# Optimization experiments

Measured on AMD Instinct MI355X. Metric: run time of the kernel, lower is better.

Reference implementation:

```python
import jax, jax.numpy as jnp
import numpy as np

N = 8192
TD, ID, D = 768, 1024, 1024
E = 8
GH = D // 2  # gate hidden
EPS = 1e-5


def _init_linear(key, fan_in, shape):
    # torch nn.Linear default init: U(-1/sqrt(fan_in), 1/sqrt(fan_in))
    bound = 1.0 / np.sqrt(fan_in)
    return jax.random.uniform(key, shape, jnp.float32, -bound, bound)


def setup_inputs() -> dict:
    key = jax.random.key(0)
    ks = jax.random.split(key, 16)
    return {
        "text_features": jax.random.normal(ks[0], (N, TD), jnp.float32),
        "image_features": jax.random.normal(ks[1], (N, ID), jnp.float32),
        "Wt": _init_linear(ks[2], TD, (TD, D)),
        "bt": _init_linear(ks[3], TD, (D,)),
        "Wi": _init_linear(ks[4], ID, (ID, D)),
        "bi": _init_linear(ks[5], ID, (D,)),
        "eW1": _init_linear(ks[6], 2 * D, (E, 2 * D, D)),
        "eb1": _init_linear(ks[7], 2 * D, (E, D)),
        "eW2": _init_linear(ks[8], D, (E, D, D)),
        "eb2": _init_linear(ks[9], D, (E, D)),
        "ln_g": jnp.ones((E, D), jnp.float32),
        "ln_b": jnp.zeros((E, D), jnp.float32),
        "gW1": _init_linear(ks[10], 2 * D, (2 * D, GH)),
        "gb1": _init_linear(ks[11], 2 * D, (GH,)),
        "gW2": _init_linear(ks[12], GH, (GH, E)),
        "gb2": _init_linear(ks[13], GH, (E,)),
    }


def reference(text_features, image_features, Wt, bt, Wi, bi,
              eW1, eb1, eW2, eb2, ln_g, ln_b, gW1, gb1, gW2, gb2):
    # project both modalities to shared dim D (dropout is identity in eval)
    ta = text_features @ Wt + bt            # [N, D]
    ia = image_features @ Wi + bi           # [N, D]
    c = jnp.concatenate([ta, ia], axis=-1)  # [N, 2D]

    # gating MLP -> softmax over experts
    gh = jax.nn.silu(c @ gW1 + gb1)                      # [N, GH]
    w = jax.nn.softmax(gh @ gW2 + gb2, axis=-1)          # [N, E]

    # all experts densely, batched over E
    h = jax.nn.silu(jnp.einsum('nc,ecd->ned', c, eW1) + eb1)   # [N, E, D]
    o = jnp.einsum('ned,edf->nef', h, eW2) + eb2               # [N, E, D]

    # per-expert LayerNorm over last dim
    mu = o.mean(axis=-1, keepdims=True)
    var = ((o - mu) ** 2).mean(axis=-1, keepdims=True)
    o = (o - mu) * jax.lax.rsqrt(var + EPS) * ln_g + ln_b      # [N, E, D]

    # gate-weighted sum over experts
    return jnp.einsum('ned,ne->nd', o, w)                      # [N, D]
```

## Files before the change

kernel.cpp:

```cpp
#include <hip/hip_runtime.h>

#define NROWS 8192
#define TDIM 768
#define IDIM 1024
#define DDIM 1024
#define NEXP 8
#define GHID 512

typedef __attribute__((ext_vector_type(8))) short short8;
typedef __attribute__((ext_vector_type(4))) float f4;
typedef __attribute__((ext_vector_type(4))) unsigned short us4;

__device__ __forceinline__ unsigned short f2bf(float f) {
  union { float f; unsigned u; } v; v.f = f;
  unsigned r = v.u + 0x7FFF + ((v.u >> 16) & 1);
  return (unsigned short)(r >> 16);
}
__device__ __forceinline__ float bf2f(unsigned short u) {
  union { unsigned u; float f; } v; v.u = ((unsigned)u) << 16;
  return v.f;
}

__device__ __forceinline__ void gload16(const void* g, void* l) {
  __builtin_amdgcn_global_load_lds(
      (const __attribute__((address_space(1))) void*)g,
      (__attribute__((address_space(3))) void*)l, 16, 0, 0);
}

__global__ __launch_bounds__(256) void cast_bf16_kernel(
    const float* __restrict__ src, unsigned short* __restrict__ dst, int n4) {
  int i = blockIdx.x * 256 + threadIdx.x;
  if (i < n4) {
    f4 v = ((const f4*)src)[i];
    us4 o;
    o[0] = f2bf(v[0]); o[1] = f2bf(v[1]); o[2] = f2bf(v[2]); o[3] = f2bf(v[3]);
    ((us4*)dst)[i] = o;
  }
}

__global__ __launch_bounds__(256) void transpose_cast_kernel(
    const float* __restrict__ src, unsigned short* __restrict__ dst, int R, int C) {
  __shared__ float tile[32][33];
  size_t base = (size_t)blockIdx.z * R * C;
  int c0 = blockIdx.x * 32, r0 = blockIdx.y * 32;
  int tx = threadIdx.x, ty = threadIdx.y;
#pragma unroll
  for (int j = 0; j < 32; j += 8)
    tile[ty + j][tx] = src[base + (size_t)(r0 + ty + j) * C + c0 + tx];
  __syncthreads();
#pragma unroll
  for (int j = 0; j < 32; j += 8)
    dst[base + (size_t)(c0 + ty + j) * R + r0 + tx] = f2bf(tile[tx][ty + j]);
}

template <int SILU, int OUTBF>
__global__ __launch_bounds__(512, 1) void gemm256_kernel(
    const unsigned short* __restrict__ A, const unsigned short* __restrict__ BT,
    const float* __restrict__ bias, void* __restrict__ Cptr,
    int K, int lda, int ldb, int ldc,
    size_t sA, size_t sB, size_t sBias, size_t sC) {
  __shared__ __align__(16) char LDS[131072];

  const unsigned short* Ab = A + (size_t)blockIdx.z * sA;
  const unsigned short* Bb = BT + (size_t)blockIdx.z * sB;
  const float* biasb = bias + (size_t)blockIdx.z * sBias;

  const int gx = gridDim.x;
  const int nwg = gx * gridDim.y;
  const int orig = blockIdx.y * gx + blockIdx.x;
  const int q = nwg >> 3, r = nwg & 7;
  const int xcd = orig & 7, idx = orig >> 3;
  const int wgid = (xcd < r ? xcd * (q + 1) : r * (q + 1) + (xcd - r) * q) + idx;
  const int bx = wgid % gx, by = wgid / gx;

  const int tid = threadIdx.x;
  const int wave = tid >> 6, lane = tid & 63;
  const int wm = wave >> 2, wn = wave & 3;
  const int row0 = by * 256, col0 = bx * 256;

  f4 acc[8][4] = {};

  const int srow = tid >> 3;
  const int scolg = ((tid & 7) << 4) ^ (((tid >> 3) & 7) << 4);
  const size_t lda2 = (size_t)lda * 2, ldb2 = (size_t)ldb * 2;
  const char* Abytes = (const char*)Ab;
  const char* Bbytes = (const char*)Bb;
  const size_t aG = (size_t)(row0 + srow) * lda2 + scolg;
  const size_t bG = (size_t)(col0 + srow) * ldb2 + scolg;
  char* ldsw = LDS + wave * 1024;

  const int aBase = (wm * 128 + (lane & 15)) * 128;
  const int bBase = 32768 + (wn * 64 + (lane & 15)) * 128;
  const int ck0 = ((lane >> 4) << 4) ^ ((lane & 7) << 4);

  const int NT = K >> 6;

#pragma unroll
  for (int p = 0; p < 4; p++)
    gload16(Abytes + aG + (size_t)(p * 64) * lda2, ldsw + p * 8192);
#pragma unroll
  for (int p = 0; p < 4; p++)
    gload16(Bbytes + bG + (size_t)(p * 64) * ldb2, ldsw + 32768 + p * 8192);

  short8 bv[4][2];
  for (int t = 0; t < NT; t++) {
    const int buf = (t & 1) << 16;
    const int nbuf = 65536 - buf;
    const size_t kb = (size_t)(t + 1) << 7;
    const bool more = (t + 1 < NT);

    if (more) {
      gload16(Abytes + aG + kb, ldsw + nbuf);
      gload16(Abytes + aG + (size_t)64 * lda2 + kb, ldsw + nbuf + 8192);
      asm volatile("s_waitcnt vmcnt(2)" ::: "memory");
    } else {
      asm volatile("s_waitcnt vmcnt(0)" ::: "memory");
    }
    __builtin_amdgcn_s_barrier();
    __builtin_amdgcn_sched_barrier(0);
    {
      short8 av[2][2];
#pragma unroll
      for (int n = 0; n < 4; n++)
#pragma unroll
        for (int kk = 0; kk < 2; kk++)
          bv[n][kk] = *(const short8*)(LDS + buf + bBase + n * 2048 + (ck0 ^ (kk << 6)));
#pragma unroll
      for (int m = 0; m < 2; m++)
#pragma unroll
        for (int kk = 0; kk < 2; kk++)
          av[m][kk] = *(const short8*)(LDS + buf + aBase + m * 2048 + (ck0 ^ (kk << 6)));
      asm volatile("s_waitcnt lgkmcnt(0)" ::: "memory");
      __builtin_amdgcn_sched_barrier(0);
      __builtin_amdgcn_s_setprio(1);
#pragma unroll
      for (int kk = 0; kk < 2; kk++)
#pragma unroll
        for (int m = 0; m < 2; m++)
#pragma unroll
          for (int n = 0; n < 4; n++)
            acc[m][n] = __builtin_amdgcn_mfma_f32_16x16x32_bf16(av[m][kk], bv[n][kk], acc[m][n], 0, 0, 0);
      __builtin_amdgcn_s_setprio(0);
    }
    __builtin_amdgcn_s_barrier();

#pragma unroll
    for (int ph = 1; ph < 4; ph++) {
      if (more) {
        if (ph == 1) {
          gload16(Abytes + aG + (size_t)128 * lda2 + kb, ldsw + nbuf + 16384);
          gload16(Abytes + aG + (size_t)192 * lda2 + kb, ldsw + nbuf + 24576);
        } else if (ph == 2) {
          gload16(Bbytes + bG + kb, ldsw + nbuf + 32768);
          gload16(Bbytes + bG + (size_t)64 * ldb2 + kb, ldsw + nbuf + 40960);
        } else {
          gload16(Bbytes + bG + (size_t)128 * ldb2 + kb, ldsw + nbuf + 49152);
          gload16(Bbytes + bG + (size_t)192 * ldb2 + kb, ldsw + nbuf + 57344);
        }
      }
      short8 av[2][2];
#pragma unroll
      for (int m = 0; m < 2; m++)
#pragma unroll
        for (int kk = 0; kk < 2; kk++)
          av[m][kk] = *(const short8*)(LDS + buf + aBase + (ph * 2 + m) * 2048 + (ck0 ^ (kk << 6)));
      asm volatile("s_waitcnt lgkmcnt(0)" ::: "memory");
      __builtin_amdgcn_sched_barrier(0);
      __builtin_amdgcn_s_setprio(1);
#pragma unroll
      for (int kk = 0; kk < 2; kk++)
#pragma unroll
        for (int m = 0; m < 2; m++)
#pragma unroll
          for (int n = 0; n < 4; n++)
            acc[ph * 2 + m][n] = __builtin_amdgcn_mfma_f32_16x16x32_bf16(av[m][kk], bv[n][kk], acc[ph * 2 + m][n], 0, 0, 0);
      __builtin_amdgcn_s_setprio(0);
      __builtin_amdgcn_s_barrier();
    }
  }

  const int crow0 = row0 + wm * 128 + (lane >> 4) * 4;
  const int ccol0 = col0 + wn * 64 + (lane & 15);
  char* Cb = (char*)Cptr + (size_t)blockIdx.z * sC * (OUTBF ? 2 : 4);
#pragma unroll
  for (int n = 0; n < 4; n++) {
    const int col = ccol0 + n * 16;
    const float bvv = biasb[col];
#pragma unroll
    for (int m = 0; m < 8; m++) {
#pragma unroll
      for (int r2 = 0; r2 < 4; r2++) {
        float v = acc[m][n][r2] + bvv;
        if (SILU) v = v / (1.0f + __expf(-v));
        const size_t cidx = (size_t)(crow0 + m * 16 + r2) * ldc + col;
        if (OUTBF) ((unsigned short*)Cb)[cidx] = f2bf(v);
        else       ((float*)Cb)[cidx] = v;
      }
    }
  }
}

template <int SILU, int OUTBF>
__global__ __launch_bounds__(256) void gemm_tn_kernel(
    const unsigned short* __restrict__ A, const unsigned short* __restrict__ BT,
    const float* __restrict__ bias, void* __restrict__ Cptr,
    int K, int lda, int ldb, int ldc,
    size_t sA, size_t sB, size_t sBias, size_t sC) {
  __shared__ unsigned short Als[128 * 32];
  __shared__ unsigned short Bls[128 * 32];

  const unsigned short* Ab = A + (size_t)blockIdx.z * sA;
  const unsigned short* Bb = BT + (size_t)blockIdx.z * sB;
  const float* biasb = bias + (size_t)blockIdx.z * sBias;

  const int gx = gridDim.x;
  const int nwg = gx * gridDim.y;
  const int orig = blockIdx.y * gx + blockIdx.x;
  const int q = nwg >> 3, r = nwg & 7;
  const int xcd = orig & 7, idx = orig >> 3;
  const int wgid = (xcd < r ? xcd * (q + 1) : r * (q + 1) + (xcd - r) * q) + idx;
  const int bx = wgid % gx, by = wgid / gx;

  const int tid = threadIdx.x;
  const int wave = tid >> 6, lane = tid & 63;
  const int row0 = by * 128, col0 = bx * 128;
  const int wm = wave >> 1, wn = wave & 1;
  f4 acc[4][4] = {};

  const int aoff = (wm * 64 + (lane & 15)) * 32 + (lane >> 4) * 8;
  const int boff = (wn * 64 + (lane & 15)) * 32 + (lane >> 4) * 8;

  const int L0 = tid, L1 = tid + 256;
  const size_t aofs0 = (size_t)(row0 + (L0 >> 2)) * lda + (L0 & 3) * 8;
  const size_t aofs1 = (size_t)(row0 + (L1 >> 2)) * lda + (L1 & 3) * 8;
  const size_t bofs0 = (size_t)(col0 + (L0 >> 2)) * ldb + (L0 & 3) * 8;
  const size_t bofs1 = (size_t)(col0 + (L1 >> 2)) * ldb + (L1 & 3) * 8;
  char* abase0 = (char*)Als + wave * 1024;
  char* abase1 = (char*)Als + 4096 + wave * 1024;
  char* bbase0 = (char*)Bls + wave * 1024;
  char* bbase1 = (char*)Bls + 4096 + wave * 1024;

  for (int k0 = 0; k0 < K; k0 += 32) {
    gload16(Ab + aofs0 + k0, abase0);
    gload16(Ab + aofs1 + k0, abase1);
    gload16(Bb + bofs0 + k0, bbase0);
    gload16(Bb + bofs1 + k0, bbase1);
    __syncthreads();
    short8 af[4], bfr[4];
#pragma unroll
    for (int i = 0; i < 4; i++) af[i] = *(const short8*)&Als[aoff + i * 512];
#pragma unroll
    for (int j = 0; j < 4; j++) bfr[j] = *(const short8*)&Bls[boff + j * 512];
#pragma unroll
    for (int i = 0; i < 4; i++)
#pragma unroll
      for (int j = 0; j < 4; j++)
        acc[i][j] = __builtin_amdgcn_mfma_f32_16x16x32_bf16(af[i], bfr[j], acc[i][j], 0, 0, 0);
    __syncthreads();
  }

  const int crow = row0 + wm * 64 + (lane >> 4) * 4;
  const int ccol = col0 + wn * 64 + (lane & 15);
  char* Cb = (char*)Cptr + (size_t)blockIdx.z * sC * (OUTBF ? 2 : 4);
#pragma unroll
  for (int j = 0; j < 4; j++) {
    const int col = ccol + j * 16;
    const float bv = biasb[col];
#pragma unroll
    for (int i = 0; i < 4; i++) {
#pragma unroll
      for (int r2 = 0; r2 < 4; r2++) {
        float v = acc[i][j][r2] + bv;
        if (SILU) v = v / (1.0f + __expf(-v));
        const size_t cidx = (size_t)(crow + i * 16 + r2) * ldc + col;
        if (OUTBF)
          ((unsigned short*)Cb)[cidx] = f2bf(v);
        else
          ((float*)Cb)[cidx] = v;
      }
    }
  }
}

__global__ __launch_bounds__(256) void gate_kernel(
    const unsigned short* __restrict__ gh, const float* __restrict__ gW2,
    const float* __restrict__ gb2, float* __restrict__ wout) {
  __shared__ float sW[NEXP * GHID];
  int tid = threadIdx.x;
  for (int i = tid; i < GHID * NEXP; i += 256) {
    int k = i >> 3, e = i & 7;
    sW[e * GHID + k] = gW2[i];
  }
  __syncthreads();
  int wave = tid >> 6, lane = tid & 63;
  int row = blockIdx.x * 4 + wave;
  float acc[NEXP] = {};
#pragma unroll
  for (int i = 0; i < 8; i++) {
    int k = lane + 64 * i;
    float x = bf2f(gh[(size_t)row * GHID + k]);
#pragma unroll
    for (int e = 0; e < NEXP; e++) acc[e] += x * sW[e * GHID + k];
  }
#pragma unroll
  for (int off = 32; off; off >>= 1)
#pragma unroll
    for (int e = 0; e < NEXP; e++) acc[e] += __shfl_xor(acc[e], off);
  float lg[NEXP], mx = -1e30f;
#pragma unroll
  for (int e = 0; e < NEXP; e++) { lg[e] = acc[e] + gb2[e]; mx = fmaxf(mx, lg[e]); }
  float s = 0.f;
#pragma unroll
  for (int e = 0; e < NEXP; e++) { lg[e] = __expf(lg[e] - mx); s += lg[e]; }
  if (lane < NEXP) wout[(size_t)row * NEXP + lane] = lg[lane] / s;
}

__global__ __launch_bounds__(256) void ln_acc8_kernel(
    const float* __restrict__ o, const float* __restrict__ wgate,
    const float* __restrict__ ln_g, const float* __restrict__ ln_b,
    float* __restrict__ out, int row0) {
  int wave = threadIdx.x >> 6, lane = threadIdx.x & 63;
  int lrow = blockIdx.x * 4 + wave;
  int grow = row0 + lrow;
  float res[16];
#pragma unroll
  for (int u = 0; u < 16; u++) res[u] = 0.f;
#pragma unroll
  for (int e = 0; e < NEXP; e++) {
    const float* orow = o + (size_t)lrow * (NEXP * DDIM) + (size_t)e * DDIM;
    float xs[16];
    float s = 0.f, s2 = 0.f;
#pragma unroll
    for (int qq = 0; qq < 4; qq++) {
      f4 t = *(const f4*)&orow[qq * 256 + lane * 4];
#pragma unroll
      for (int u = 0; u < 4; u++) {
        xs[qq * 4 + u] = t[u];
        s += t[u];
        s2 += t[u] * t[u];
      }
    }
#pragma unroll
    for (int off = 32; off; off >>= 1) {
      s += __shfl_xor(s, off);
      s2 += __shfl_xor(s2, off);
    }
    const float inv = 1.0f / 1024.0f;
    float mu = s * inv;
    float var = s2 * inv - mu * mu;
    float rr = rsqrtf(var + 1e-5f);
    float wv = wgate[(size_t)grow * NEXP + e];
#pragma unroll
    for (int qq = 0; qq < 4; qq++) {
      int d = qq * 256 + lane * 4;
      f4 gg = *(const f4*)&ln_g[(size_t)e * DDIM + d];
      f4 bb = *(const f4*)&ln_b[(size_t)e * DDIM + d];
#pragma unroll
      for (int u = 0; u < 4; u++)
        res[qq * 4 + u] += wv * ((xs[qq * 4 + u] - mu) * rr * gg[u] + bb[u]);
    }
  }
  size_t rowbase = (size_t)grow * DDIM;
#pragma unroll
  for (int qq = 0; qq < 4; qq++) {
    f4 t;
#pragma unroll
    for (int u = 0; u < 4; u++) t[u] = res[qq * 4 + u];
    *(f4*)&out[rowbase + qq * 256 + lane * 4] = t;
  }
}

extern "C" void kernel_launch(void* const* d_in, const int* in_sizes, int n_in,
                              void* d_out, int out_size, void* d_ws, size_t ws_size,
                              hipStream_t stream) {
  const float* text  = (const float*)d_in[0];
  const float* image = (const float*)d_in[1];
  const float* Wt    = (const float*)d_in[2];
  const float* bt    = (const float*)d_in[3];
  const float* Wi    = (const float*)d_in[4];
  const float* bi    = (const float*)d_in[5];
  const float* eW1   = (const float*)d_in[6];
  const float* eb1   = (const float*)d_in[7];
  const float* eW2   = (const float*)d_in[8];
  const float* eb2   = (const float*)d_in[9];
  const float* ln_g  = (const float*)d_in[10];
  const float* ln_b  = (const float*)d_in[11];
  const float* gW1   = (const float*)d_in[12];
  const float* gb1   = (const float*)d_in[13];
  const float* gW2   = (const float*)d_in[14];
  const float* gb2   = (const float*)d_in[15];
  float* out = (float*)d_out;

  size_t off = 0;
  auto alloc = [&](size_t bytes) -> void* {
    void* p = (char*)d_ws + off;
    off += (bytes + 255) & ~(size_t)255;
    return p;
  };
  unsigned short* eW1T = (unsigned short*)alloc((size_t)NEXP * 2 * DDIM * DDIM * 2);
  unsigned short* eW2T = (unsigned short*)alloc((size_t)NEXP * DDIM * DDIM * 2);
  unsigned short* c_bf = (unsigned short*)alloc((size_t)NROWS * 2 * DDIM * 2);
  float* wgate         = (float*)alloc((size_t)NROWS * NEXP * 4);
  const size_t overlay0 = off;

  unsigned short* text_bf = (unsigned short*)alloc((size_t)NROWS * TDIM * 2);
  unsigned short* img_bf  = (unsigned short*)alloc((size_t)NROWS * IDIM * 2);
  unsigned short* WtT     = (unsigned short*)alloc((size_t)TDIM * DDIM * 2);
  unsigned short* WiT     = (unsigned short*)alloc((size_t)IDIM * DDIM * 2);
  unsigned short* gW1T    = (unsigned short*)alloc((size_t)2 * DDIM * GHID * 2);
  unsigned short* gh_bf   = (unsigned short*)alloc((size_t)NROWS * GHID * 2);

  int slab = 8192;
  while (slab > 256 &&
         overlay0 + (size_t)slab * (size_t)(2 * NEXP * DDIM + 4 * NEXP * DDIM) > ws_size)
    slab >>= 1;
  unsigned short* h_slab = (unsigned short*)((char*)d_ws + overlay0);
  float* o_slab = (float*)((char*)d_ws + overlay0 + (size_t)slab * NEXP * DDIM * 2);

  cast_bf16_kernel<<<(NROWS * TDIM / 4 + 255) / 256, 256, 0, stream>>>(text, text_bf, NROWS * TDIM / 4);
  cast_bf16_kernel<<<(NROWS * IDIM / 4 + 255) / 256, 256, 0, stream>>>(image, img_bf, NROWS * IDIM / 4);

  transpose_cast_kernel<<<dim3(DDIM / 32, TDIM / 32, 1), dim3(32, 8), 0, stream>>>(Wt, WtT, TDIM, DDIM);
  transpose_cast_kernel<<<dim3(DDIM / 32, IDIM / 32, 1), dim3(32, 8), 0, stream>>>(Wi, WiT, IDIM, DDIM);
  transpose_cast_kernel<<<dim3(GHID / 32, 2 * DDIM / 32, 1), dim3(32, 8), 0, stream>>>(gW1, gW1T, 2 * DDIM, GHID);
  transpose_cast_kernel<<<dim3(DDIM / 32, 2 * DDIM / 32, NEXP), dim3(32, 8), 0, stream>>>(eW1, eW1T, 2 * DDIM, DDIM);
  transpose_cast_kernel<<<dim3(DDIM / 32, DDIM / 32, NEXP), dim3(32, 8), 0, stream>>>(eW2, eW2T, DDIM, DDIM);

  gemm_tn_kernel<0, 1><<<dim3(DDIM / 128, NROWS / 128), 256, 0, stream>>>(
      text_bf, WtT, bt, c_bf, TDIM, TDIM, TDIM, 2 * DDIM, 0, 0, 0, 0);
  gemm_tn_kernel<0, 1><<<dim3(DDIM / 128, NROWS / 128), 256, 0, stream>>>(
      img_bf, WiT, bi, c_bf + DDIM, IDIM, IDIM, IDIM, 2 * DDIM, 0, 0, 0, 0);

  gemm_tn_kernel<1, 1><<<dim3(GHID / 128, NROWS / 128), 256, 0, stream>>>(
      c_bf, gW1T, gb1, gh_bf, 2 * DDIM, 2 * DDIM, 2 * DDIM, GHID, 0, 0, 0, 0);

  gate_kernel<<<NROWS / 4, 256, 0, stream>>>(gh_bf, gW2, gb2, wgate);

  for (int r0 = 0; r0 < NROWS; r0 += slab) {
    gemm256_kernel<1, 1><<<dim3(NEXP * DDIM / 256, slab / 256), 512, 0, stream>>>(
        c_bf + (size_t)r0 * 2 * DDIM, eW1T, eb1, h_slab,
        2 * DDIM, 2 * DDIM, 2 * DDIM, NEXP * DDIM, 0, 0, 0, 0);
    gemm256_kernel<0, 0><<<dim3(DDIM / 256, slab / 256, NEXP), 512, 0, stream>>>(
        h_slab, eW2T, eb2, o_slab,
        DDIM, NEXP * DDIM, DDIM, NEXP * DDIM,
        (size_t)DDIM, (size_t)DDIM * DDIM, (size_t)DDIM, (size_t)DDIM);
    ln_acc8_kernel<<<slab / 4, 256, 0, stream>>>(o_slab, wgate, ln_g, ln_b, out, r0);
  }
}
```

Before: 719.3 us.

## Prefetch B tiles two k-steps ahead and restage GEMM LDS pipeline

Restructures the GEMM main loop's global-to-LDS prefetch schedule. B tiles are now loaded two k-iterations ahead and A tiles one ahead. Each load is issued right after the LDS fragment reads of its phase, and the per-iteration vmcnt wait moves to the end of the last phase. This aims to hide global load latency and remove the stall at the top of each iteration, at the cost of a more intricate barrier and waitcnt ordering, which risks buffer overwrite hazards.

Measured after the change: 731.7 us. About the same (+1.7%).

```diff
diff --git a/kernel.cpp b/kernel.cpp
--- a/kernel.cpp
+++ b/kernel.cpp
@@ -89,47 +89,61 @@
   const size_t bG = (size_t)(col0 + srow) * ldb2 + scolg;
   char* ldsw = LDS + wave * 1024;
 
+  auto stageA0 = [&](int tt) {
+    const size_t kb = (size_t)tt << 7;
+    char* d = ldsw + ((tt & 1) << 16);
+    gload16(Abytes + aG + kb, d);
+    gload16(Abytes + aG + (size_t)64 * lda2 + kb, d + 8192);
+  };
+  auto stageA1 = [&](int tt) {
+    const size_t kb = (size_t)tt << 7;
+    char* d = ldsw + ((tt & 1) << 16);
+    gload16(Abytes + aG + (size_t)128 * lda2 + kb, d + 16384);
+    gload16(Abytes + aG + (size_t)192 * lda2 + kb, d + 24576);
+  };
+  auto stageB0 = [&](int tt) {
+    const size_t kb = (size_t)tt << 7;
+    char* d = ldsw + ((tt & 1) << 16) + 32768;
+    gload16(Bbytes + bG + kb, d);
+    gload16(Bbytes + bG + (size_t)64 * ldb2 + kb, d + 8192);
+  };
+  auto stageB1 = [&](int tt) {
+    const size_t kb = (size_t)tt << 7;
+    char* d = ldsw + ((tt & 1) << 16) + 32768;
+    gload16(Bbytes + bG + (size_t)128 * ldb2 + kb, d + 16384);
+    gload16(Bbytes + bG + (size_t)192 * ldb2 + kb, d + 24576);
+  };
+
   const int aBase = (wm * 128 + (lane & 15)) * 128;
   const int bBase = 32768 + (wn * 64 + (lane & 15)) * 128;
   const int ck0 = ((lane >> 4) << 4) ^ ((lane & 7) << 4);
 
   const int NT = K >> 6;
 
-#pragma unroll
-  for (int p = 0; p < 4; p++)
-    gload16(Abytes + aG + (size_t)(p * 64) * lda2, ldsw + p * 8192);
-#pragma unroll
-  for (int p = 0; p < 4; p++)
-    gload16(Bbytes + bG + (size_t)(p * 64) * ldb2, ldsw + 32768 + p * 8192);
+  stageA0(0); stageA1(0); stageB0(0); stageB1(0);
+  if (NT > 1) { stageB0(1); stageB1(1); }
+  asm volatile("s_waitcnt vmcnt(4)" ::: "memory");
+  __builtin_amdgcn_s_barrier();
 
   short8 bv[4][2];
   for (int t = 0; t < NT; t++) {
-    const int buf = (t & 1) << 16;
-    const int nbuf = 65536 - buf;
-    const size_t kb = (size_t)(t + 1) << 7;
-    const bool more = (t + 1 < NT);
-
-    if (more) {
-      gload16(Abytes + aG + kb, ldsw + nbuf);
-      gload16(Abytes + aG + (size_t)64 * lda2 + kb, ldsw + nbuf + 8192);
-      asm volatile("s_waitcnt vmcnt(2)" ::: "memory");
-    } else {
-      asm volatile("s_waitcnt vmcnt(0)" ::: "memory");
-    }
-    __builtin_amdgcn_s_barrier();
-    __builtin_amdgcn_sched_barrier(0);
+    const int aB = ((t & 1) << 16) + aBase;
+    const int bB = ((t & 1) << 16) + bBase;
+
     {
       short8 av[2][2];
 #pragma unroll
       for (int n = 0; n < 4; n++)
 #pragma unroll
         for (int kk = 0; kk < 2; kk++)
-          bv[n][kk] = *(const short8*)(LDS + buf + bBase + n * 2048 + (ck0 ^ (kk << 6)));
+          bv[n][kk] = *(const short8*)(LDS + bB + n * 2048 + (ck0 ^ (kk << 6)));
 #pragma unroll
       for (int m = 0; m < 2; m++)
 #pragma unroll
         for (int kk = 0; kk < 2; kk++)
-          av[m][kk] = *(const short8*)(LDS + buf + aBase + m * 2048 + (ck0 ^ (kk << 6)));
+          av[m][kk] = *(const short8*)(LDS + aB + m * 2048 + (ck0 ^ (kk << 6)));
+      if (t + 1 < NT) stageA0(t + 1);
+      __builtin_amdgcn_s_barrier();
       asm volatile("s_waitcnt lgkmcnt(0)" ::: "memory");
       __builtin_amdgcn_sched_barrier(0);
       __builtin_amdgcn_s_setprio(1);
@@ -141,29 +155,24 @@
           for (int n = 0; n < 4; n++)
             acc[m][n] = __builtin_amdgcn_mfma_f32_16x16x32_bf16(av[m][kk], bv[n][kk], acc[m][n], 0, 0, 0);
       __builtin_amdgcn_s_setprio(0);
-    }
-    __builtin_amdgcn_s_barrier();
+      __builtin_amdgcn_s_barrier();
+    }
 
 #pragma unroll
     for (int ph = 1; ph < 4; ph++) {
-      if (more) {
-        if (ph == 1) {
-          gload16(Abytes + aG + (size_t)128 * lda2 + kb, ldsw + nbuf + 16384);
-          gload16(Abytes + aG + (size_t)192 * lda2 + kb, ldsw + nbuf + 24576);
-        } else if (ph == 2) {
-          gload16(Bbytes + bG + kb, ldsw + nbuf + 32768);
-          gload16(Bbytes + bG + (size_t)64 * ldb2 + kb, ldsw + nbuf + 40960);
-        } else {
-          gload16(Bbytes + bG + (size_t)128 * ldb2 + kb, ldsw + nbuf + 49152);
-          gload16(Bbytes + bG + (size_t)192 * ldb2 + kb, ldsw + nbuf + 57344);
-        }
+      short8 av[2][2];
+#pragma unroll
+      for (int m = 0; m < 2; m++)
+#pragma unroll
+        for (int kk = 0; kk < 2; kk++)
+          av[m][kk] = *(const short8*)(LDS + aB + (ph * 2 + m) * 2048 + (ck0 ^ (kk << 6)));
+      if (ph == 1) {
+        if (t + 1 < NT) stageA1(t + 1);
+        if (t + 2 < NT) stageB0(t + 2);
+      } else if (ph == 2) {
+        if (t + 2 < NT) stageB1(t + 2);
       }
-      short8 av[2][2];
-#pragma unroll
-      for (int m = 0; m < 2; m++)
-#pragma unroll
-        for (int kk = 0; kk < 2; kk++)
-          av[m][kk] = *(const short8*)(LDS + buf + aBase + (ph * 2 + m) * 2048 + (ck0 ^ (kk << 6)));
+      __builtin_amdgcn_s_barrier();
       asm volatile("s_waitcnt lgkmcnt(0)" ::: "memory");
       __builtin_amdgcn_sched_barrier(0);
       __builtin_amdgcn_s_setprio(1);
@@ -175,6 +184,13 @@
           for (int n = 0; n < 4; n++)
             acc[ph * 2 + m][n] = __builtin_amdgcn_mfma_f32_16x16x32_bf16(av[m][kk], bv[n][kk], acc[ph * 2 + m][n], 0, 0, 0);
       __builtin_amdgcn_s_setprio(0);
+      if (ph == 3) {
+        if (t + 2 < NT) {
+          asm volatile("s_waitcnt vmcnt(4)" ::: "memory");
+        } else if (t + 1 < NT) {
+          asm volatile("s_waitcnt vmcnt(0)" ::: "memory");
+        }
+      }
       __builtin_amdgcn_s_barrier();
     }
   }
```
